# Optimization experiments

Hardware: AMD Instinct MI355X
Metric: run time of the kernel (lower is better)

## Reference

```python
import jax, jax.numpy as jnp
import numpy as np
from jax import lax

# Module config (mirrors init_kwargs)
N, CIN, COUT, H, W = 16, 512, 512, 64, 64
KS = 3          # conv kernel_size
FACTOR = 2
GAIN = 1.0
LRMUL = 1.0
FIR_1D = np.array([1.0, 3.0, 3.0, 1.0], dtype=np.float32)

# upfirdn pad amounts as in the torch code
FIRN = 4
P = FIRN - FACTOR + (KS - 1)      # = 4
PAD0 = (P + 1) // 2               # = 2
PAD1 = P // 2                     # = 2
W_LRMUL = GAIN / np.sqrt(CIN * COUT * KS * KS)  # he_std * lrmul (use_wscale)
B_LRMUL = LRMUL
SQRT2 = np.float32(np.sqrt(2.0))


def setup_inputs() -> dict:
    key = jax.random.key(0)
    kx, kw, kb = jax.random.split(key, 3)
    x = jax.random.normal(kx, (N, CIN, H, W), dtype=jnp.float32)
    # weight init: randn * init_std, init_std = 1/lrmul = 1.0 under use_wscale
    weight = jax.random.normal(kw, (COUT, CIN, KS, KS), dtype=jnp.float32)
    bias = jax.random.normal(kb, (COUT,), dtype=jnp.float32) * 0.1
    kf = np.outer(FIR_1D, FIR_1D)
    kf = kf / kf.sum() * GAIN
    fir = jnp.asarray(kf, dtype=jnp.float32)  # [4,4], non-trainable
    return {"x": x, "weight": weight, "bias": bias, "fir": fir}


def _blur_and_resize(x, fir):
    # x: [N, C, H, W]; FIR blur via depthwise trick: fold C into batch.
    n, c, h, w = x.shape
    y = x.reshape(n * c, 1, h, w)
    y = jnp.pad(y, ((0, 0), (0, 0), (PAD0, PAD1), (PAD0, PAD1)))
    # valid conv with 4x4 FIR -> [n*c, 1, h+1, w+1]
    y = lax.conv_general_dilated(
        y, fir[None, None, :, :], window_strides=(1, 1), padding="VALID",
        dimension_numbers=("NCHW", "OIHW", "NCHW"))
    # F.interpolate(mode='nearest') from (h+1, w+1) back to (h, w):
    # torch nearest uses src = floor(dst * in/out) == (dst*(h+1))//h
    ri = (jnp.arange(h) * (h + 1)) // h
    ci = (jnp.arange(w) * (w + 1)) // w
    y = y[:, :, ri, :][:, :, :, ci]
    return y.reshape(n, c, h, w)


def reference(x, weight, bias, fir):
    y = _blur_and_resize(x, fir)
    # strided conv: stride=factor, padding=ks//2 (SAME-ish), cross-correlation
    out = lax.conv_general_dilated(
        y, weight * W_LRMUL, window_strides=(FACTOR, FACTOR),
        padding=[(KS // 2, KS // 2), (KS // 2, KS // 2)],
        dimension_numbers=("NCHW", "OIHW", "NCHW"))
    out = out + (bias * B_LRMUL)[None, :, None, None]
    out = jnp.where(out >= 0, out, 0.2 * out) * SQRT2  # leaky_relu(0.2) * sqrt(2)
    return out
```

## Files before the change

### kernel.cpp

```cpp
#include <hip/hip_runtime.h>
#include <hip/hip_bf16.h>
#include <stdint.h>

#define N_IMG 16
#define C_IN  512
#define C_OUT 512
#define H_IN  64
#define W_IN  64
#define OH    32
#define OW    32
#define PIX   (N_IMG*OH*OW)

#define YPH 65
#define YPW 33

#define W2_ELEMS (9*C_OUT*C_IN)
#define W2_BYTES (W2_ELEMS*2)

typedef __attribute__((ext_vector_type(8))) __bf16 bf16x8;
typedef __attribute__((ext_vector_type(4))) float  f32x4;

__device__ inline void gload_lds16(const void* g, void* l) {
  __builtin_amdgcn_global_load_lds(
      (const __attribute__((address_space(1))) void*)g,
      (__attribute__((address_space(3))) void*)l, 16, 0, 0);
}

__global__ __launch_bounds__(256) void prep_w_kernel(const float* __restrict__ w,
                                                     __hip_bfloat16* __restrict__ w2) {
  int id = blockIdx.x * 256 + threadIdx.x;
  const float* p = w + (size_t)id * 9;
  float v[9];
#pragma unroll
  for (int t = 0; t < 9; ++t) v[t] = p[t] * (1.0f/1536.0f);
#pragma unroll
  for (int t = 0; t < 9; ++t)
    w2[(size_t)t*(C_OUT*C_IN) + id] = __float2bfloat16(v[t]);
}

__global__ __launch_bounds__(256) void blur_kernel(const float* __restrict__ x,
                                                   __hip_bfloat16* __restrict__ yt) {
  __shared__ float obuf[2][32][65];
  const int tid = threadIdx.x;
  const int c   = tid >> 3;
  const int p8  = tid & 7;
  const int w8  = p8 * 8;
  const int r0  = blockIdx.x * 8;
  const int cib = blockIdx.y;
  const int n   = blockIdx.z;
  const float* xc = x + ((size_t)(n*C_IN + cib*32 + c) * H_IN) * W_IN + w8;

  {
    const uint4 z4 = {0u, 0u, 0u, 0u};
    if (tid < 16) {
      int hh  = r0 + (tid >> 1);
      int par = tid & 1;
      size_t slot = (((size_t)n*YPH + hh + 1)*2 + par)*YPW;
      uint4* p = (uint4*)(yt + slot*C_IN + cib*32);
      p[0]=z4; p[1]=z4; p[2]=z4; p[3]=z4;
    }
    if (blockIdx.x == 0 && tid < 66) {
      int par = tid / 33;
      int cc  = tid - par*33;
      size_t slot = ((size_t)n*YPH*2 + par)*YPW + cc;
      uint4* p = (uint4*)(yt + slot*C_IN + cib*32);
      p[0]=z4; p[1]=z4; p[2]=z4; p[3]=z4;
    }
  }

  const int rp_oc  = tid & 3;
  const int rp_p   = tid >> 2;
  const int rp_par = rp_p & 1;
  const int rp_ch  = rp_p >> 1;

  float cur[8], nxt[8];
  float h1[8], h2[8], h3[8];
#pragma unroll
  for (int j = 0; j < 8; ++j) { h1[j] = 0.f; h2[j] = 0.f; h3[j] = 0.f; }

  auto load_row = [&](int r, float* dst) {
    if (r >= 0 && r < H_IN) {
      const float4 a = *(const float4*)(xc + (size_t)r * W_IN);
      const float4 b = *(const float4*)(xc + (size_t)r * W_IN + 4);
      dst[0]=a.x; dst[1]=a.y; dst[2]=a.z; dst[3]=a.w;
      dst[4]=b.x; dst[5]=b.y; dst[6]=b.z; dst[7]=b.w;
    } else {
#pragma unroll
      for (int j = 0; j < 8; ++j) dst[j] = 0.f;
    }
  };

  load_row(r0 - 2, cur);
  for (int ri = 0; ri < 11; ++ri) {
    const int r = r0 - 2 + ri;
    if (ri < 10) load_row(r + 1, nxt);

    float l2 = __shfl_up(cur[6], 1);
    float l1 = __shfl_up(cur[7], 1);
    float rr = __shfl_down(cur[0], 1);
    if (p8 == 0) { l2 = 0.f; l1 = 0.f; }
    if (p8 == 7) { rr = 0.f; }
    float hc[8];
    hc[0] = l2 + 3.f*(l1 + cur[0]) + cur[1];
    hc[1] = l1 + 3.f*(cur[0] + cur[1]) + cur[2];
#pragma unroll
    for (int j = 2; j < 7; ++j) hc[j] = cur[j-2] + 3.f*(cur[j-1] + cur[j]) + cur[j+1];
    hc[7] = cur[5] + 3.f*(cur[6] + cur[7]) + rr;

    if (ri >= 3) {
      const int h = r - 1;
      const int b = ri & 1;
#pragma unroll
      for (int j = 0; j < 8; ++j)
        obuf[b][c][w8 + j] = (h3[j] + 3.f*(h2[j] + h1[j]) + hc[j]) * (1.0f/64.0f);
      __syncthreads();
      alignas(16) __hip_bfloat16 t16[8];
#pragma unroll
      for (int j = 0; j < 8; ++j)
        t16[j] = __float2bfloat16(obuf[b][rp_oc*8 + j][rp_p]);
      size_t slot = ((size_t)(n*YPH + h + 1)*2 + rp_par)*YPW + rp_ch + 1;
      *(uint4*)(yt + slot*C_IN + cib*32 + rp_oc*8) = *(uint4*)t16;
    }

#pragma unroll
    for (int j = 0; j < 8; ++j) {
      h3[j] = h2[j]; h2[j] = h1[j]; h1[j] = hc[j]; cur[j] = nxt[j];
    }
  }
}

#define ABYTES (128*64*2)
__global__ __launch_bounds__(256, 2) void conv_kernel(const __hip_bfloat16* __restrict__ w2,
                            const __hip_bfloat16* __restrict__ yt,
                            const float* __restrict__ bias,
                            float* __restrict__ out) {
  __shared__ __hip_bfloat16 Alds[2][128*64];
  __shared__ __hip_bfloat16 Blds[2][128*64];
  const int tid  = threadIdx.x;
  const int lane = tid & 63;
  const int wv   = tid >> 6;
  const int wm   = wv & 1;
  const int wn   = wv >> 1;
  const int cob0 = blockIdx.y * 128;
  const int pixb = blockIdx.x * 128;
  const int quad = lane >> 4;
  const int wvb  = tid & 192;

  size_t aoff[4];
  int    bseg8[4], bn65[4], boh2[4], bow_[4];
  int    ldsOff[4];
#pragma unroll
  for (int i = 0; i < 4; ++i) {
    int s = i*256 + tid;
    int r = s >> 3;
    int pp = s & 7;
    int gg = pp ^ (r & 7);
    aoff[i] = (size_t)(cob0 + r)*C_IN + gg*8;
    int gp = pixb + r;
    bn65[i] = (gp >> 10) * YPH;
    boh2[i] = ((gp >> 5) & 31) * 2;
    bow_[i] = gp & 31;
    bseg8[i] = gg*8;
    ldsOff[i] = (i*256 + wvb)*16;
  }

  auto stage = [&](int c, int b) {
    const int t   = c >> 3;
    const int cib = (c & 7) << 6;
    const int kh  = (t * 11) >> 5;
    const int kw  = t - kh*3;
    const int par = (kw == 1) ? 0 : 1;
    const int d   = (kw == 0) ? 0 : 1;
    const __hip_bfloat16* wt = w2 + (size_t)t * (C_OUT*C_IN) + cib;
#pragma unroll
    for (int i = 0; i < 4; ++i)
      gload_lds16(wt + aoff[i], (char*)Alds + b*ABYTES + ldsOff[i]);
#pragma unroll
    for (int i = 0; i < 4; ++i) {
      size_t slot = ((size_t)(bn65[i] + boh2[i] + kh)*2 + par)*YPW + bow_[i] + d;
      gload_lds16(yt + slot*C_IN + bseg8[i] + cib, (char*)Blds + b*ABYTES + ldsOff[i]);
    }
  };

  f32x4 acc[4][4];
  const f32x4 zero = {0.f, 0.f, 0.f, 0.f};
#pragma unroll
  for (int mi = 0; mi < 4; ++mi)
#pragma unroll
    for (int ni = 0; ni < 4; ++ni) acc[mi][ni] = zero;

  stage(0, 0);
#pragma unroll 2
  for (int cch = 0; cch < 72; ++cch) {
    __syncthreads();
    if (cch < 71) stage(cch + 1, (cch + 1) & 1);
    const int b = cch & 1;
    const char* Ab = (const char*)Alds + b*ABYTES;
    const char* Bb = (const char*)Blds + b*ABYTES;
#pragma unroll
    for (int kk = 0; kk < 2; ++kk) {
      bf16x8 af[4], bfr[4];
#pragma unroll
      for (int mi = 0; mi < 4; ++mi) {
        int r = wm*64 + mi*16 + (lane & 15);
        int gsg = kk*4 + quad;
        af[mi] = *(const bf16x8*)(Ab + r*128 + ((gsg ^ (r & 7))*16));
      }
#pragma unroll
      for (int ni = 0; ni < 4; ++ni) {
        int r = wn*64 + ni*16 + (lane & 15);
        int gsg = kk*4 + quad;
        bfr[ni] = *(const bf16x8*)(Bb + r*128 + ((gsg ^ (r & 7))*16));
      }
#pragma unroll
      for (int mi = 0; mi < 4; ++mi)
#pragma unroll
        for (int ni = 0; ni < 4; ++ni)
          acc[mi][ni] = __builtin_amdgcn_mfma_f32_16x16x32_bf16(af[mi], bfr[ni], acc[mi][ni], 0, 0, 0);
    }
  }

#pragma unroll
  for (int mi = 0; mi < 4; ++mi) {
#pragma unroll
    for (int reg = 0; reg < 4; ++reg) {
      int co = cob0 + wm*64 + mi*16 + quad*4 + reg;
      float bv = bias[co];
#pragma unroll
      for (int ni = 0; ni < 4; ++ni) {
        int gp  = pixb + wn*64 + ni*16 + (lane & 15);
        int n   = gp >> 10;
        int ohw = gp & 1023;
        float v = acc[mi][ni][reg] + bv;
        v = (v >= 0.f ? v : 0.2f*v) * 1.41421356f;
        out[(((size_t)n*C_OUT + co) << 10) + ohw] = v;
      }
    }
  }
}

extern "C" void kernel_launch(void* const* d_in, const int* in_sizes, int n_in,
                              void* d_out, int out_size, void* d_ws, size_t ws_size,
                              hipStream_t stream) {
  const float* x    = (const float*)d_in[0];
  const float* w    = (const float*)d_in[1];
  const float* bias = (const float*)d_in[2];
  float* out = (float*)d_out;
  __hip_bfloat16* w2 = (__hip_bfloat16*)d_ws;
  __hip_bfloat16* yt = (__hip_bfloat16*)((char*)d_ws + W2_BYTES);

  prep_w_kernel<<<(C_OUT*C_IN)/256, 256, 0, stream>>>(w, w2);
  blur_kernel<<<dim3(8, 16, 16), 256, 0, stream>>>(x, yt);
  conv_kernel<<<dim3(PIX/128, C_OUT/128), 256, 0, stream>>>(w2, yt, bias, out);
}
```

Baseline: 306.1 us.

## Enlarge conv tile to 128x256 with 8 waves and triple-buffered LDS pipeline

The implicit-GEMM conv kernel now uses 512-thread blocks with a 128x256 output tile, giving 8 waves in a 2x4 layout, each still computing 64x64. LDS goes from double to triple buffering, with prefetch two K-steps ahead. Each step is split into two half-MFMA phases that interleave global-to-LDS staging, using explicit vmcnt/lgkmcnt waits, raw barriers and setprio. The aim is better operand reuse and more overlap of loads with MFMA work, at the cost of 144KB of dynamic LDS, more barriers per step, and only half as many blocks in the grid.

```diff
diff --git a/kernel.cpp b/kernel.cpp
--- a/kernel.cpp
+++ b/kernel.cpp
@@ -17,6 +17,15 @@
 #define W2_ELEMS (9*C_OUT*C_IN)
 #define W2_BYTES (W2_ELEMS*2)
 
+#define BM 128
+#define BN 256
+#define BK 64
+#define NKT 72
+#define ATILE_B (BM*BK*2)
+#define BTILE_B (BN*BK*2)
+#define BUF_B   (ATILE_B+BTILE_B)
+#define LDS_TOTAL (3*BUF_B)
+
 typedef __attribute__((ext_vector_type(8))) __bf16 bf16x8;
 typedef __attribute__((ext_vector_type(4))) float  f32x4;
 
@@ -25,6 +34,18 @@
       (const __attribute__((address_space(1))) void*)g,
       (__attribute__((address_space(3))) void*)l, 16, 0, 0);
 }
+
+#define WAIT_VM(N) asm volatile("s_waitcnt vmcnt(" #N ")" ::: "memory")
+#define WAIT_LGKM0 asm volatile("s_waitcnt lgkmcnt(0)" ::: "memory")
+__device__ inline void barrier_raw() {
+  asm volatile("" ::: "memory");
+  __builtin_amdgcn_s_barrier();
+  asm volatile("" ::: "memory");
+}
+
+struct TagMain  { static constexpr bool stg = true;  static constexpr int vn = 6;  };
+struct TagTail0 { static constexpr bool stg = false; static constexpr int vn = 0;  };
+struct TagTail1 { static constexpr bool stg = false; static constexpr int vn = -1; };
 
 __global__ __launch_bounds__(256) void prep_w_kernel(const float* __restrict__ w,
                                                      __hip_bfloat16* __restrict__ w2) {
@@ -129,57 +150,79 @@
   }
 }
 
-#define ABYTES (128*64*2)
-__global__ __launch_bounds__(256, 2) void conv_kernel(const __hip_bfloat16* __restrict__ w2,
+__global__ __launch_bounds__(512, 2) void conv_kernel(const __hip_bfloat16* __restrict__ w2,
                             const __hip_bfloat16* __restrict__ yt,
                             const float* __restrict__ bias,
                             float* __restrict__ out) {
-  __shared__ __hip_bfloat16 Alds[2][128*64];
-  __shared__ __hip_bfloat16 Blds[2][128*64];
-  const int tid  = threadIdx.x;
-  const int lane = tid & 63;
-  const int wv   = tid >> 6;
-  const int wm   = wv & 1;
-  const int wn   = wv >> 1;
-  const int cob0 = blockIdx.y * 128;
-  const int pixb = blockIdx.x * 128;
-  const int quad = lane >> 4;
-  const int wvb  = tid & 192;
-
-  size_t aoff[4];
-  int    bseg8[4], bn65[4], boh2[4], bow_[4];
-  int    ldsOff[4];
+  extern __shared__ char lds[];
+  const int tid   = threadIdx.x;
+  const int lane  = tid & 63;
+  const int wv    = tid >> 6;
+  const int wvb64 = wv * 64;
+  const int wm    = wv & 1;
+  const int wn    = wv >> 1;
+  const int cob0  = blockIdx.y * BM;
+  const int pixb  = blockIdx.x * BN;
+  const int quad  = lane >> 4;
+
+  size_t aoff[2];
+#pragma unroll
+  for (int i = 0; i < 2; ++i) {
+    int s = i*512 + tid, r = s >> 3, p = s & 7, g = p ^ (r & 7);
+    aoff[i] = (size_t)(cob0 + r)*C_IN + g*8;
+  }
+  int bn65[4], boh2[4], bow_[4], bseg8[4];
 #pragma unroll
   for (int i = 0; i < 4; ++i) {
-    int s = i*256 + tid;
-    int r = s >> 3;
-    int pp = s & 7;
-    int gg = pp ^ (r & 7);
-    aoff[i] = (size_t)(cob0 + r)*C_IN + gg*8;
+    int s = i*512 + tid, r = s >> 3, p = s & 7, g = p ^ (r & 7);
     int gp = pixb + r;
-    bn65[i] = (gp >> 10) * YPH;
-    boh2[i] = ((gp >> 5) & 31) * 2;
-    bow_[i] = gp & 31;
-    bseg8[i] = gg*8;
-    ldsOff[i] = (i*256 + wvb)*16;
-  }
-
-  auto stage = [&](int c, int b) {
-    const int t   = c >> 3;
-    const int cib = (c & 7) << 6;
-    const int kh  = (t * 11) >> 5;
-    const int kw  = t - kh*3;
-    const int par = (kw == 1) ? 0 : 1;
-    const int d   = (kw == 0) ? 0 : 1;
-    const __hip_bfloat16* wt = w2 + (size_t)t * (C_OUT*C_IN) + cib;
-#pragma unroll
-    for (int i = 0; i < 4; ++i)
-      gload_lds16(wt + aoff[i], (char*)Alds + b*ABYTES + ldsOff[i]);
-#pragma unroll
-    for (int i = 0; i < 4; ++i) {
-      size_t slot = ((size_t)(bn65[i] + boh2[i] + kh)*2 + par)*YPW + bow_[i] + d;
-      gload_lds16(yt + slot*C_IN + bseg8[i] + cib, (char*)Blds + b*ABYTES + ldsOff[i]);
-    }
+    bn65[i]  = (gp >> 10) * YPH;
+    boh2[i]  = ((gp >> 5) & 31) * 2;
+    bow_[i]  = gp & 31;
+    bseg8[i] = g*8;
+  }
+
+  int aRdOff[4][2], bRdOff[4][2];
+#pragma unroll
+  for (int f = 0; f < 4; ++f) {
+    int ra = wm*64 + f*16 + (lane & 15);
+    int rb = wn*64 + f*16 + (lane & 15);
+#pragma unroll
+    for (int kk = 0; kk < 2; ++kk) {
+      aRdOff[f][kk] = ra*128 + (((kk*4 + quad) ^ (ra & 7)) * 16);
+      bRdOff[f][kk] = rb*128 + (((kk*4 + quad) ^ (rb & 7)) * 16);
+    }
+  }
+
+  struct BP { int kh, par, d, cib; };
+  auto bparams = [&](int kt) {
+    const int t  = kt >> 3;
+    const int kh = (t * 11) >> 5;
+    const int kw = t - kh*3;
+    BP r; r.kh = kh; r.par = (kw == 1) ? 0 : 1; r.d = (kw == 0) ? 0 : 1;
+    r.cib = (kt & 7) << 6;
+    return r;
+  };
+  auto stageA = [&](int kt, int b) {
+    const int t = kt >> 3;
+    const __hip_bfloat16* wt = w2 + (size_t)t*(C_OUT*C_IN) + ((kt & 7) << 6);
+    char* da = lds + b*BUF_B;
+    gload_lds16(wt + aoff[0], da + (size_t)(      wvb64)*16);
+    gload_lds16(wt + aoff[1], da + (size_t)(512 + wvb64)*16);
+  };
+  auto stageB01 = [&](BP bp, int b) {
+    char* db = lds + b*BUF_B + ATILE_B;
+    size_t s0 = ((size_t)(bn65[0] + boh2[0] + bp.kh)*2 + bp.par)*YPW + bow_[0] + bp.d;
+    gload_lds16(yt + s0*C_IN + bseg8[0] + bp.cib, db + (size_t)(      wvb64)*16);
+    size_t s1 = ((size_t)(bn65[1] + boh2[1] + bp.kh)*2 + bp.par)*YPW + bow_[1] + bp.d;
+    gload_lds16(yt + s1*C_IN + bseg8[1] + bp.cib, db + (size_t)(512 + wvb64)*16);
+  };
+  auto stageB23 = [&](BP bp, int b) {
+    char* db = lds + b*BUF_B + ATILE_B;
+    size_t s2 = ((size_t)(bn65[2] + boh2[2] + bp.kh)*2 + bp.par)*YPW + bow_[2] + bp.d;
+    gload_lds16(yt + s2*C_IN + bseg8[2] + bp.cib, db + (size_t)(1024 + wvb64)*16);
+    size_t s3 = ((size_t)(bn65[3] + boh2[3] + bp.kh)*2 + bp.par)*YPW + bow_[3] + bp.d;
+    gload_lds16(yt + s3*C_IN + bseg8[3] + bp.cib, db + (size_t)(1536 + wvb64)*16);
   };
 
   f32x4 acc[4][4];
@@ -189,36 +232,81 @@
 #pragma unroll
     for (int ni = 0; ni < 4; ++ni) acc[mi][ni] = zero;
 
-  stage(0, 0);
-#pragma unroll 2
-  for (int cch = 0; cch < 72; ++cch) {
-    __syncthreads();
-    if (cch < 71) stage(cch + 1, (cch + 1) & 1);
-    const int b = cch & 1;
-    const char* Ab = (const char*)Alds + b*ABYTES;
-    const char* Bb = (const char*)Blds + b*ABYTES;
+  {
+    BP b0 = bparams(0);
+    stageA(0, 0); stageB01(b0, 0); stageB23(b0, 0);
+    BP b1 = bparams(1);
+    stageA(1, 1); stageB01(b1, 1); stageB23(b1, 1);
+    WAIT_VM(6);
+    barrier_raw();
+  }
+
+  auto body = [&](int k, int cb, int sb, auto tag) {
+    using T = decltype(tag);
+    const char* Ab = lds + cb*BUF_B;
+    const char* Bb = Ab + ATILE_B;
+    BP bp{};
+    if constexpr (T::stg) bp = bparams(k + 2);
+
+    bf16x8 af[4][2], b0[2], b1[2];
+#pragma unroll
+    for (int mi = 0; mi < 4; ++mi)
+#pragma unroll
+      for (int kk = 0; kk < 2; ++kk)
+        af[mi][kk] = *(const bf16x8*)(Ab + aRdOff[mi][kk]);
 #pragma unroll
     for (int kk = 0; kk < 2; ++kk) {
-      bf16x8 af[4], bfr[4];
+      b0[kk] = *(const bf16x8*)(Bb + bRdOff[0][kk]);
+      b1[kk] = *(const bf16x8*)(Bb + bRdOff[1][kk]);
+    }
+    if constexpr (T::stg) { stageA(k + 2, sb); stageB01(bp, sb); }
+    barrier_raw();
+    WAIT_LGKM0;
+    __builtin_amdgcn_sched_barrier(0);
+    __builtin_amdgcn_s_setprio(1);
+#pragma unroll
+    for (int kk = 0; kk < 2; ++kk)
 #pragma unroll
       for (int mi = 0; mi < 4; ++mi) {
-        int r = wm*64 + mi*16 + (lane & 15);
-        int gsg = kk*4 + quad;
-        af[mi] = *(const bf16x8*)(Ab + r*128 + ((gsg ^ (r & 7))*16));
+        acc[mi][0] = __builtin_amdgcn_mfma_f32_16x16x32_bf16(af[mi][kk], b0[kk], acc[mi][0], 0, 0, 0);
+        acc[mi][1] = __builtin_amdgcn_mfma_f32_16x16x32_bf16(af[mi][kk], b1[kk], acc[mi][1], 0, 0, 0);
       }
-#pragma unroll
-      for (int ni = 0; ni < 4; ++ni) {
-        int r = wn*64 + ni*16 + (lane & 15);
-        int gsg = kk*4 + quad;
-        bfr[ni] = *(const bf16x8*)(Bb + r*128 + ((gsg ^ (r & 7))*16));
+    __builtin_amdgcn_s_setprio(0);
+    barrier_raw();
+
+    bf16x8 b2[2], b3[2];
+#pragma unroll
+    for (int kk = 0; kk < 2; ++kk) {
+      b2[kk] = *(const bf16x8*)(Bb + bRdOff[2][kk]);
+      b3[kk] = *(const bf16x8*)(Bb + bRdOff[3][kk]);
+    }
+    if constexpr (T::stg) stageB23(bp, sb);
+    if constexpr (T::vn == 6) WAIT_VM(6);
+    else if constexpr (T::vn == 0) WAIT_VM(0);
+    barrier_raw();
+    WAIT_LGKM0;
+    __builtin_amdgcn_sched_barrier(0);
+    __builtin_amdgcn_s_setprio(1);
+#pragma unroll
+    for (int kk = 0; kk < 2; ++kk)
+#pragma unroll
+      for (int mi = 0; mi < 4; ++mi) {
+        acc[mi][2] = __builtin_amdgcn_mfma_f32_16x16x32_bf16(af[mi][kk], b2[kk], acc[mi][2], 0, 0, 0);
+        acc[mi][3] = __builtin_amdgcn_mfma_f32_16x16x32_bf16(af[mi][kk], b3[kk], acc[mi][3], 0, 0, 0);
       }
-#pragma unroll
-      for (int mi = 0; mi < 4; ++mi)
-#pragma unroll
-        for (int ni = 0; ni < 4; ++ni)
-          acc[mi][ni] = __builtin_amdgcn_mfma_f32_16x16x32_bf16(af[mi], bfr[ni], acc[mi][ni], 0, 0, 0);
-    }
-  }
+    __builtin_amdgcn_s_setprio(0);
+    barrier_raw();
+  };
+
+  int cb = 0, sb = 2;
+  for (int k = 0; k < NKT - 2; ++k) {
+    body(k, cb, sb, TagMain{});
+    cb = (cb == 2) ? 0 : cb + 1;
+    sb = (sb == 2) ? 0 : sb + 1;
+  }
+  body(NKT - 2, cb, sb, TagTail0{});
+  cb = (cb == 2) ? 0 : cb + 1;
+  body(NKT - 1, cb, 0, TagTail1{});
 
 #pragma unroll
   for (int mi = 0; mi < 4; ++mi) {
@@ -249,7 +337,14 @@
   __hip_bfloat16* w2 = (__hip_bfloat16*)d_ws;
   __hip_bfloat16* yt = (__hip_bfloat16*)((char*)d_ws + W2_BYTES);
 
+  static bool attr_set = false;
+  if (!attr_set) {
+    hipFuncSetAttribute(reinterpret_cast<const void*>(conv_kernel),
+                        hipFuncAttributeMaxDynamicSharedMemorySize, LDS_TOTAL);
+    attr_set = true;
+  }
+
   prep_w_kernel<<<(C_OUT*C_IN)/256, 256, 0, stream>>>(w, w2);
   blur_kernel<<<dim3(8, 16, 16), 256, 0, stream>>>(x, yt);
-  conv_kernel<<<dim3(PIX/128, C_OUT/128), 256, 0, stream>>>(w2, yt, bias, out);
-}
+  conv_kernel<<<dim3(PIX/BN, C_OUT/BM), 512, LDS_TOTAL, stream>>>(w2, yt, bias, out);
+}
```

Result: no change. 306.7 us (+0.2%).
